# Optimization experiments

Hardware: AMD Instinct MI355X
Metric: run time of the kernel (lower is better)

## Reference

```python
import jax, jax.numpy as jnp
import numpy as np

B, P, D, A = 256, 196, 512, 512

def setup_inputs() -> dict:
    key = jax.random.key(0)
    ks = jax.random.split(key, 12)
    sc = 1.0 / np.sqrt(D)
    sa = 1.0 / np.sqrt(A)
    return {
        "encoder_out": jax.random.normal(ks[0], (B, P, D), jnp.float32),
        "decoder_hidden": jax.random.normal(ks[1], (B, D), jnp.float32),
        "st": jax.random.normal(ks[2], (B, D), jnp.float32),
        "Wv": jax.random.normal(ks[3], (D, A), jnp.float32) * sc,
        "bv": jnp.zeros((A,), jnp.float32),
        "Wh": jax.random.normal(ks[4], (D, A), jnp.float32) * sc,
        "bh": jnp.zeros((A,), jnp.float32),
        "Ws": jax.random.normal(ks[5], (D, A), jnp.float32) * sc,
        "bs": jnp.zeros((A,), jnp.float32),
        "Wav": jax.random.normal(ks[6], (A,), jnp.float32) * sa,
        "bav": jnp.zeros((), jnp.float32),
        "Was": jax.random.normal(ks[7], (A,), jnp.float32) * sa,
        "bas": jnp.zeros((), jnp.float32),
    }

def reference(encoder_out, decoder_hidden, st, Wv, bv, Wh, bh, Ws, bs, Wav, bav, Was, bas):
    # hidden: (B, A)
    hidden = decoder_hidden @ Wh + bh
    # v: (B, P, A)
    v = jnp.einsum('bpd,da->bpa', encoder_out, Wv) + bv
    # z_t: (B, P) -- additive attention scores over pixels
    z_t = jnp.einsum('bpa,a->bp', jnp.tanh(v + hidden[:, None, :]), Wav) + bav
    alpha_t = jax.nn.softmax(z_t, axis=1)
    # c_t: (B, D) -- attention-weighted encoding
    c_t = jnp.einsum('bpd,bp->bd', encoder_out, alpha_t)
    # sentinel branch: s (B, A), s_att (B, 1)
    s = st @ Ws + bs
    s_att = jnp.tanh(s + hidden) @ Was + bas  # (B,)
    z_t_extended = jnp.concatenate([z_t, s_att[:, None]], axis=1)  # (B, P+1)
    alpha_t_hat = jax.nn.softmax(z_t_extended, axis=1)
    beta_t = alpha_t_hat[:, -1:]  # (B, 1)
    c_hat_t = beta_t * st + (1.0 - beta_t) * c_t
    return (c_hat_t, alpha_t, beta_t)
```

## Files before the change

kernel.cpp:

```cpp
#include <hip/hip_runtime.h>
#include <hip/hip_bf16.h>
#include <cstdint>

#define B_ 256
#define P_ 196
#define D_ 512
#define A_ 512

#define OUT_CHAT  0
#define OUT_ALPHA (B_*D_)
#define OUT_BETA  (B_*D_ + B_*P_)

typedef unsigned short ushort_t;
typedef uint32_t u32;
typedef uint64_t u64;
typedef __attribute__((ext_vector_type(8))) __bf16 bf16x8;
typedef __attribute__((ext_vector_type(4))) float f32x4;

__device__ __forceinline__ ushort_t f2bf(float f) {
    union { float f; u32 i; } v; v.f = f;
    u32 r = (v.i + 0x7fffu + ((v.i >> 16) & 1u)) >> 16;
    return (ushort_t)r;
}
__device__ __forceinline__ float bfbits2f(u32 lo16) {
    union { u32 i; float f; } v; v.i = lo16 << 16; return v.f;
}
__device__ __forceinline__ u32 cvt2bf(float x, float y) {
    union { __hip_bfloat162 h; u32 u; } v;
    v.h = __float22bfloat162_rn(make_float2(x, y));
    return v.u;
}
__device__ __forceinline__ float tanh_fast(float x) {
    float e = __expf(2.0f * x);
    return 1.0f - 2.0f / (e + 1.0f);
}
__device__ __forceinline__ void async_load16(const ushort_t* g, ushort_t* l) {
    __builtin_amdgcn_global_load_lds(
        (const __attribute__((address_space(1))) unsigned int*)g,
        (__attribute__((address_space(3))) unsigned int*)l, 16, 0, 0);
}

__global__ __launch_bounds__(256) void k_prep(
    const float* __restrict__ E, const float* __restrict__ dh,
    const float* __restrict__ st,
    const float* __restrict__ Wv, const float* __restrict__ Wh,
    const float* __restrict__ Ws,
    ushort_t* __restrict__ Ebf, ushort_t* __restrict__ dhbf,
    ushort_t* __restrict__ stbf,
    ushort_t* __restrict__ WvT, ushort_t* __restrict__ WhT,
    ushort_t* __restrict__ WsT)
{
    __shared__ ushort_t tile[32][33];
    int bx = blockIdx.x;
    if (bx < 12544) {
        size_t i0 = (size_t)bx * 512 + threadIdx.x;
        const float4* src = (const float4*)E;
        u64* dst = (u64*)Ebf;
        float4 v0 = src[i0];
        float4 v1 = src[i0 + 256];
        dst[i0]       = (u64)cvt2bf(v0.x, v0.y) | ((u64)cvt2bf(v0.z, v0.w) << 32);
        dst[i0 + 256] = (u64)cvt2bf(v1.x, v1.y) | ((u64)cvt2bf(v1.z, v1.w) << 32);
    } else if (bx < 12672) {
        int gid = (bx - 12544) * 256 + threadIdx.x;
        float4 dv = ((const float4*)dh)[gid];
        float4 sv = ((const float4*)st)[gid];
        ((u64*)dhbf)[gid] = (u64)cvt2bf(dv.x, dv.y) | ((u64)cvt2bf(dv.z, dv.w) << 32);
        ((u64*)stbf)[gid] = (u64)cvt2bf(sv.x, sv.y) | ((u64)cvt2bf(sv.z, sv.w) << 32);
    } else {
        int idx = bx - 12672;
        int z   = idx >> 8;
        int rem = idx & 255;
        int tby = rem >> 4, tbx = rem & 15;
        const float* W  = (z == 0) ? Wv  : (z == 1) ? Wh  : Ws;
        ushort_t*    WT = (z == 0) ? WvT : (z == 1) ? WhT : WsT;
        int t = threadIdx.x, r = t >> 5, c = t & 31;
#pragma unroll
        for (int i = 0; i < 4; ++i) {
            int row = r + 8 * i;
            tile[row][c] = f2bf(W[(size_t)(tby * 32 + row) * A_ + tbx * 32 + c]);
        }
        __syncthreads();
#pragma unroll
        for (int i = 0; i < 4; ++i) {
            int row = r + 8 * i;
            WT[(size_t)(tbx * 32 + row) * D_ + tby * 32 + c] = tile[c][row];
        }
    }
}

#define PADK 72

__global__ __launch_bounds__(256) void k1_mfma(
    const ushort_t* __restrict__ dhbf, const ushort_t* __restrict__ stbf,
    const ushort_t* __restrict__ WhT,  const ushort_t* __restrict__ WsT,
    const float* __restrict__ bh, const float* __restrict__ bs,
    float* __restrict__ hidden_ws, float* __restrict__ s_ws)
{
    __shared__ ushort_t As[128 * PADK];
    __shared__ ushort_t Bs[128 * PADK];

    int mat = blockIdx.z;
    const ushort_t* Abf = mat ? stbf : dhbf;
    const ushort_t* WT  = mat ? WsT  : WhT;
    const float*    bia = mat ? bs   : bh;
    float*          outp = mat ? s_ws : hidden_ws;

    int tid = threadIdx.x;
    int m0 = blockIdx.y * 128;
    int n0 = blockIdx.x * 128;

    int lane = tid & 63, w = tid >> 6;
    int wm = w & 1, wn = w >> 1;
    int col = lane & 15, q = lane >> 4;

    f32x4 acc[4][4];
#pragma unroll
    for (int tm = 0; tm < 4; ++tm)
#pragma unroll
        for (int tn = 0; tn < 4; ++tn)
            acc[tm][tn] = (f32x4){0.f, 0.f, 0.f, 0.f};

    const ushort_t* arow = As + (wm * 64 + col) * PADK + q * 8;
    const ushort_t* brow = Bs + (wn * 64 + col) * PADK + q * 8;

    int sr = tid >> 3, sc = tid & 7;
    for (int kt = 0; kt < D_ / 64; ++kt) {
#pragma unroll
        for (int i = 0; i < 4; ++i) {
            int row = sr + i * 32;
            *(uint4*)(As + row * PADK + sc * 8) =
                *(const uint4*)(Abf + (size_t)(m0 + row) * D_ + kt * 64 + sc * 8);
            *(uint4*)(Bs + row * PADK + sc * 8) =
                *(const uint4*)(WT + (size_t)(n0 + row) * D_ + kt * 64 + sc * 8);
        }
        __syncthreads();
#pragma unroll
        for (int ks = 0; ks < 2; ++ks) {
            bf16x8 afr[4];
#pragma unroll
            for (int tm = 0; tm < 4; ++tm)
                afr[tm] = *(const bf16x8*)(arow + tm * 16 * PADK + ks * 32);
#pragma unroll
            for (int tn = 0; tn < 4; ++tn) {
                bf16x8 bfr = *(const bf16x8*)(brow + tn * 16 * PADK + ks * 32);
#pragma unroll
                for (int tm = 0; tm < 4; ++tm)
                    acc[tm][tn] = __builtin_amdgcn_mfma_f32_16x16x32_bf16(
                        afr[tm], bfr, acc[tm][tn], 0, 0, 0);
            }
        }
        __syncthreads();
    }

#pragma unroll
    for (int tm = 0; tm < 4; ++tm)
#pragma unroll
        for (int r = 0; r < 4; ++r) {
            int b = m0 + wm * 64 + tm * 16 + q * 4 + r;
#pragma unroll
            for (int tn = 0; tn < 4; ++tn) {
                int n = n0 + wn * 64 + tn * 16 + col;
                outp[(size_t)b * A_ + n] = acc[tm][tn][r] + bia[n];
            }
        }
}

#define BM 128
#define BN 256
#define BKk 64
__global__ __launch_bounds__(256, 3) void k2_z_bf(
    const ushort_t* __restrict__ Ebf, const ushort_t* __restrict__ WvT,
    const float* __restrict__ hidden_ws, const float* __restrict__ bv,
    const float* __restrict__ Wav, float* __restrict__ z2_ws)
{
    __shared__ ushort_t As[BM * BKk];
    __shared__ ushort_t Bs[BN * BKk];
    __shared__ float hv_s[2][BN];
    __shared__ float wav_s[BN];
    __shared__ float zpart[2][BM];

    int tid = threadIdx.x;
    int m0  = blockIdx.x * BM;
    int n0  = blockIdx.y * BN;
    int b0  = m0 / P_;
    int b1  = (m0 + BM - 1) / P_;

    {
        int a = n0 + tid;
        float bva = bv[a];
        hv_s[0][tid] = hidden_ws[(size_t)b0 * A_ + a] + bva;
        hv_s[1][tid] = hidden_ws[(size_t)b1 * A_ + a] + bva;
        wav_s[tid]   = Wav[a];
    }

    int lane = tid & 63, w = tid >> 6;
    int wm = w & 1, wn = w >> 1;
    int col = lane & 15, q = lane >> 4;

    f32x4 acc[4][8];
#pragma unroll
    for (int tm = 0; tm < 4; ++tm)
#pragma unroll
        for (int tn = 0; tn < 8; ++tn)
            acc[tm][tn] = (f32x4){0.f, 0.f, 0.f, 0.f};

    int srow = tid >> 3, spos = tid & 7;
    int gch  = spos ^ (srow & 7);
    const ushort_t* agb = Ebf + (size_t)(m0 + srow) * D_ + gch * 8;
    const ushort_t* bgb = WvT + (size_t)(n0 + srow) * D_ + gch * 8;
    ushort_t* alb = As + tid * 8;
    ushort_t* blb = Bs + tid * 8;

    int fx = col & 7;

    for (int kt = 0; kt < D_ / BKk; ++kt) {
#pragma unroll
        for (int i = 0; i < 4; ++i)
            async_load16(agb + (size_t)i * 32 * D_ + kt * BKk, alb + i * 2048);
#pragma unroll
        for (int i = 0; i < 8; ++i)
            async_load16(bgb + (size_t)i * 32 * D_ + kt * BKk, blb + i * 2048);
        __syncthreads();
#pragma unroll
        for (int ks = 0; ks < 2; ++ks) {
            bf16x8 afr[4];
#pragma unroll
            for (int tm = 0; tm < 4; ++tm)
                afr[tm] = *(const bf16x8*)(As + (wm * 64 + tm * 16 + col) * BKk
                                              + (((ks * 4 + q) ^ fx) * 8));
#pragma unroll
            for (int tn = 0; tn < 8; ++tn) {
                bf16x8 bfr = *(const bf16x8*)(Bs + (wn * 128 + tn * 16 + col) * BKk
                                                 + (((ks * 4 + q) ^ fx) * 8));
#pragma unroll
                for (int tm = 0; tm < 4; ++tm)
                    acc[tm][tn] = __builtin_amdgcn_mfma_f32_16x16x32_bf16(
                        afr[tm], bfr, acc[tm][tn], 0, 0, 0);
            }
        }
        __syncthreads();
    }

#pragma unroll
    for (int tm = 0; tm < 4; ++tm) {
#pragma unroll
        for (int r = 0; r < 4; ++r) {
            int row = wm * 64 + tm * 16 + q * 4 + r;
            int m   = m0 + row;
            int bsel = (m / P_) - b0;
            float zr = 0.f;
#pragma unroll
            for (int tn = 0; tn < 8; ++tn) {
                int nl = wn * 128 + tn * 16 + col;
                zr += wav_s[nl] * tanh_fast(acc[tm][tn][r] + hv_s[bsel][nl]);
            }
#pragma unroll
            for (int msk = 1; msk < 16; msk <<= 1)
                zr += __shfl_xor(zr, msk, 64);
            if (col == 0) zpart[wn][row] = zr;
        }
    }
    __syncthreads();
    if (tid < BM)
        z2_ws[(size_t)blockIdx.y * (B_ * P_) + m0 + tid] =
            zpart[0][tid] + zpart[1][tid];
}

__global__ __launch_bounds__(256) void k3_softmax(
    const float* __restrict__ z2_ws, const float* __restrict__ hidden_ws,
    const float* __restrict__ s_ws, const float* __restrict__ Was,
    const float* __restrict__ bas, const float* __restrict__ bav,
    float* __restrict__ alpha_ws, float* __restrict__ beta_ws,
    float* __restrict__ out)
{
    __shared__ float red[4];
    __shared__ float bm_s, bl_s, sa_s;
    int b = blockIdx.x, t = threadIdx.x;

    {
        int a0 = t, a1 = t + 256;
        float part = Was[a0] * tanh_fast(s_ws[(size_t)b * A_ + a0] + hidden_ws[(size_t)b * A_ + a0])
                   + Was[a1] * tanh_fast(s_ws[(size_t)b * A_ + a1] + hidden_ws[(size_t)b * A_ + a1]);
#pragma unroll
        for (int o = 32; o >= 1; o >>= 1) part += __shfl_down(part, o, 64);
        if ((t & 63) == 0) red[t >> 6] = part;
        __syncthreads();
        if (t == 0) sa_s = red[0] + red[1] + red[2] + red[3] + bas[0];
        __syncthreads();
    }

    float zv = (t < P_) ? (z2_ws[(size_t)b * P_ + t]
                         + z2_ws[(size_t)(B_ * P_) + (size_t)b * P_ + t] + bav[0])
                        : -1e30f;

    float m = zv;
#pragma unroll
    for (int o = 32; o >= 1; o >>= 1) m = fmaxf(m, __shfl_xor(m, o, 64));
    if ((t & 63) == 0) red[t >> 6] = m;
    __syncthreads();
    if (t == 0) bm_s = fmaxf(fmaxf(red[0], red[1]), fmaxf(red[2], red[3]));
    __syncthreads();
    float m1 = bm_s;

    float e = (t < P_) ? __expf(zv - m1) : 0.f;
    float s = e;
#pragma unroll
    for (int o = 32; o >= 1; o >>= 1) s += __shfl_xor(s, o, 64);
    if ((t & 63) == 0) red[t >> 6] = s;
    __syncthreads();
    if (t == 0) bl_s = red[0] + red[1] + red[2] + red[3];
    __syncthreads();
    float l1 = bl_s;

    if (t < P_) {
        float alpha = e / l1;
        alpha_ws[(size_t)b * P_ + t] = alpha;
        out[OUT_ALPHA + (size_t)b * P_ + t] = alpha;
    }
    float sa = sa_s;
    float m2 = fmaxf(m1, sa);
    float l2 = __expf(m1 - m2) * l1 + __expf(sa - m2);
    float beta = __expf(sa - m2) / l2;
    if (t == 0) {
        beta_ws[b] = beta;
        out[OUT_BETA + b] = beta;
    }
}

__global__ __launch_bounds__(256) void k4_final(
    const ushort_t* __restrict__ Ebf, const float* __restrict__ st,
    const float* __restrict__ alpha_ws, const float* __restrict__ beta_ws,
    float* __restrict__ out)
{
    __shared__ float al[P_];
    int b = blockIdx.x, t = threadIdx.x;
    if (t < P_) al[t] = alpha_ws[(size_t)b * P_ + t];
    __syncthreads();
    const u32* eb = (const u32*)(Ebf + (size_t)b * P_ * D_) + t;
    float a0 = 0.f, a1 = 0.f;
#pragma unroll 4
    for (int p = 0; p < P_; ++p) {
        u32 u = eb[(size_t)p * (D_ / 2)];
        float ap = al[p];
        a0 = fmaf(ap, bfbits2f(u & 0xffffu), a0);
        a1 = fmaf(ap, bfbits2f(u >> 16), a1);
    }
    float beta = beta_ws[b];
    float2 su = *(const float2*)(st + (size_t)b * D_ + 2 * t);
    float c0 = beta * su.x + (1.f - beta) * a0;
    float c1 = beta * su.y + (1.f - beta) * a1;
    *(float2*)(out + (size_t)b * D_ + 2 * t) = make_float2(c0, c1);
}

extern "C" void kernel_launch(void* const* d_in, const int* in_sizes, int n_in,
                              void* d_out, int out_size, void* d_ws, size_t ws_size,
                              hipStream_t stream)
{
    (void)in_sizes; (void)n_in; (void)out_size; (void)ws_size;
    const float* E   = (const float*)d_in[0];
    const float* dh  = (const float*)d_in[1];
    const float* st  = (const float*)d_in[2];
    const float* Wv  = (const float*)d_in[3];
    const float* bv  = (const float*)d_in[4];
    const float* Wh  = (const float*)d_in[5];
    const float* bh  = (const float*)d_in[6];
    const float* Ws  = (const float*)d_in[7];
    const float* bs  = (const float*)d_in[8];
    const float* Wav = (const float*)d_in[9];
    const float* bav = (const float*)d_in[10];
    const float* Was = (const float*)d_in[11];
    const float* bas = (const float*)d_in[12];
    float* out = (float*)d_out;

    char* ws = (char*)d_ws;
    ushort_t* WvT     = (ushort_t*)(ws);
    ushort_t* WhT     = (ushort_t*)(ws + 524288);
    ushort_t* WsT     = (ushort_t*)(ws + 1048576);
    float*    alpha_w = (float*)(ws + 1572864);
    float*    beta_w  = (float*)(ws + 1773568);
    float*    z2_w    = (float*)(ws + 1774592);
    ushort_t* dhbf    = (ushort_t*)(ws + 2176000);
    ushort_t* stbf    = (ushort_t*)(ws + 2438144);
    float*    hidden_w= (float*)(ws + 2700288);
    float*    s_w     = (float*)(ws + 3224576);
    ushort_t* Ebf     = (ushort_t*)(ws + 3748864);

    k_prep<<<12544 + 128 + 768, 256, 0, stream>>>(E, dh, st, Wv, Wh, Ws,
                                                  Ebf, dhbf, stbf, WvT, WhT, WsT);
    k1_mfma<<<dim3(4, 2, 2), 256, 0, stream>>>(dhbf, stbf, WhT, WsT, bh, bs,
                                               hidden_w, s_w);
    k2_z_bf<<<dim3((B_ * P_) / BM, A_ / BN), 256, 0, stream>>>(
        Ebf, WvT, hidden_w, bv, Wav, z2_w);
    k3_softmax<<<256, 256, 0, stream>>>(z2_w, hidden_w, s_w, Was, bas, bav,
                                        alpha_w, beta_w, out);
    k4_final<<<256, 256, 0, stream>>>(Ebf, st, alpha_w, beta_w, out);
}
```

Before: 258.8 us.

## Fuse softmax and context kernels, vectorize context loads, swizzle GEMM block order

Merges the softmax and weighted-context kernels into one 512-thread kernel that keeps alpha in shared memory. The alpha and beta round-trip through workspace and one launch go away. The context reduction now splits pixels across eight waves, each lane loading 16-byte chunks of bf16 rows, with a cross-wave reduction through shared memory. The GEMM kernel is also remapped to a 1D grid that interleaves the two N-halves of each M tile, aiming for better L2 reuse of the encoder rows.

```diff
diff --git a/kernel.cpp b/kernel.cpp
--- a/kernel.cpp
+++ b/kernel.cpp
@@ -38,6 +38,16 @@
     __builtin_amdgcn_global_load_lds(
         (const __attribute__((address_space(1))) unsigned int*)g,
         (__attribute__((address_space(3))) unsigned int*)l, 16, 0, 0);
+}
+__device__ __forceinline__ void fma8(float ap, uint4 v, float ac[8]) {
+    ac[0] = fmaf(ap, bfbits2f(v.x & 0xffffu), ac[0]);
+    ac[1] = fmaf(ap, bfbits2f(v.x >> 16),     ac[1]);
+    ac[2] = fmaf(ap, bfbits2f(v.y & 0xffffu), ac[2]);
+    ac[3] = fmaf(ap, bfbits2f(v.y >> 16),     ac[3]);
+    ac[4] = fmaf(ap, bfbits2f(v.z & 0xffffu), ac[4]);
+    ac[5] = fmaf(ap, bfbits2f(v.z >> 16),     ac[5]);
+    ac[6] = fmaf(ap, bfbits2f(v.w & 0xffffu), ac[6]);
+    ac[7] = fmaf(ap, bfbits2f(v.w >> 16),     ac[7]);
 }
 
 __global__ __launch_bounds__(256) void k_prep(
@@ -180,8 +190,11 @@
     __shared__ float zpart[2][BM];
 
     int tid = threadIdx.x;
-    int m0  = blockIdx.x * BM;
-    int n0  = blockIdx.y * BN;
+    int bx  = blockIdx.x;
+    int m_idx = ((bx >> 4) << 3) + (bx & 7);
+    int half  = (bx >> 3) & 1;
+    int m0  = m_idx * BM;
+    int n0  = half * BN;
     int b0  = m0 / P_;
     int b1  = (m0 + BM - 1) / P_;
 
@@ -262,94 +275,103 @@
     }
     __syncthreads();
     if (tid < BM)
-        z2_ws[(size_t)blockIdx.y * (B_ * P_) + m0 + tid] =
+        z2_ws[(size_t)half * (B_ * P_) + m0 + tid] =
             zpart[0][tid] + zpart[1][tid];
 }
 
-__global__ __launch_bounds__(256) void k3_softmax(
+__global__ __launch_bounds__(512) void k34_softmax_ct(
+    const ushort_t* __restrict__ Ebf, const float* __restrict__ st,
     const float* __restrict__ z2_ws, const float* __restrict__ hidden_ws,
     const float* __restrict__ s_ws, const float* __restrict__ Was,
     const float* __restrict__ bas, const float* __restrict__ bav,
-    float* __restrict__ alpha_ws, float* __restrict__ beta_ws,
     float* __restrict__ out)
 {
-    __shared__ float red[4];
+    __shared__ float red[8];
+    __shared__ float al[P_];
+    __shared__ float acc_s[8][516];
     __shared__ float bm_s, bl_s, sa_s;
+
     int b = blockIdx.x, t = threadIdx.x;
-
-    {
-        int a0 = t, a1 = t + 256;
-        float part = Was[a0] * tanh_fast(s_ws[(size_t)b * A_ + a0] + hidden_ws[(size_t)b * A_ + a0])
-                   + Was[a1] * tanh_fast(s_ws[(size_t)b * A_ + a1] + hidden_ws[(size_t)b * A_ + a1]);
-#pragma unroll
-        for (int o = 32; o >= 1; o >>= 1) part += __shfl_down(part, o, 64);
-        if ((t & 63) == 0) red[t >> 6] = part;
-        __syncthreads();
-        if (t == 0) sa_s = red[0] + red[1] + red[2] + red[3] + bas[0];
-        __syncthreads();
-    }
+    int lane = t & 63, w = t >> 6;
+
+    float part = Was[t] * tanh_fast(s_ws[(size_t)b * A_ + t]
+                                  + hidden_ws[(size_t)b * A_ + t]);
+#pragma unroll
+    for (int o = 32; o >= 1; o >>= 1) part += __shfl_down(part, o, 64);
+    if (lane == 0) red[w] = part;
+    __syncthreads();
+    if (t == 0) {
+        float s = 0.f;
+#pragma unroll
+        for (int i = 0; i < 8; ++i) s += red[i];
+        sa_s = s + bas[0];
+    }
+    __syncthreads();
 
     float zv = (t < P_) ? (z2_ws[(size_t)b * P_ + t]
                          + z2_ws[(size_t)(B_ * P_) + (size_t)b * P_ + t] + bav[0])
                         : -1e30f;
-
     float m = zv;
 #pragma unroll
     for (int o = 32; o >= 1; o >>= 1) m = fmaxf(m, __shfl_xor(m, o, 64));
-    if ((t & 63) == 0) red[t >> 6] = m;
-    __syncthreads();
-    if (t == 0) bm_s = fmaxf(fmaxf(red[0], red[1]), fmaxf(red[2], red[3]));
+    if (lane == 0) red[w] = m;
+    __syncthreads();
+    if (t == 0) {
+        float mm = red[0];
+#pragma unroll
+        for (int i = 1; i < 8; ++i) mm = fmaxf(mm, red[i]);
+        bm_s = mm;
+    }
     __syncthreads();
     float m1 = bm_s;
-
     float e = (t < P_) ? __expf(zv - m1) : 0.f;
     float s = e;
 #pragma unroll
     for (int o = 32; o >= 1; o >>= 1) s += __shfl_xor(s, o, 64);
-    if ((t & 63) == 0) red[t >> 6] = s;
-    __syncthreads();
-    if (t == 0) bl_s = red[0] + red[1] + red[2] + red[3];
+    if (lane == 0) red[w] = s;
+    __syncthreads();
+    if (t == 0) {
+        float ss = 0.f;
+#pragma unroll
+        for (int i = 0; i < 8; ++i) ss += red[i];
+        bl_s = ss;
+    }
     __syncthreads();
     float l1 = bl_s;
-
     if (t < P_) {
         float alpha = e / l1;
-        alpha_ws[(size_t)b * P_ + t] = alpha;
+        al[t] = alpha;
         out[OUT_ALPHA + (size_t)b * P_ + t] = alpha;
     }
     float sa = sa_s;
     float m2 = fmaxf(m1, sa);
-    float l2 = __expf(m1 - m2) * l1 + __expf(sa - m2);
-    float beta = __expf(sa - m2) / l2;
-    if (t == 0) {
-        beta_ws[b] = beta;
-        out[OUT_BETA + b] = beta;
-    }
-}
-
-__global__ __launch_bounds__(256) void k4_final(
-    const ushort_t* __restrict__ Ebf, const float* __restrict__ st,
-    const float* __restrict__ alpha_ws, const float* __restrict__ beta_ws,
-    float* __restrict__ out)
-{
-    __shared__ float al[P_];
-    int b = blockIdx.x, t = threadIdx.x;
-    if (t < P_) al[t] = alpha_ws[(size_t)b * P_ + t];
-    __syncthreads();
-    const u32* eb = (const u32*)(Ebf + (size_t)b * P_ * D_) + t;
-    float a0 = 0.f, a1 = 0.f;
+    float eb2 = __expf(sa - m2);
+    float l2 = __expf(m1 - m2) * l1 + eb2;
+    float beta = eb2 / l2;
+    if (t == 0) out[OUT_BETA + b] = beta;
+    __syncthreads();
+
+    float ac[8] = {0.f, 0.f, 0.f, 0.f, 0.f, 0.f, 0.f, 0.f};
+    const uint4* eb = (const uint4*)(Ebf + (size_t)b * P_ * D_);
 #pragma unroll 4
-    for (int p = 0; p < P_; ++p) {
-        u32 u = eb[(size_t)p * (D_ / 2)];
-        float ap = al[p];
-        a0 = fmaf(ap, bfbits2f(u & 0xffffu), a0);
-        a1 = fmaf(ap, bfbits2f(u >> 16), a1);
-    }
-    float beta = beta_ws[b];
-    float2 su = *(const float2*)(st + (size_t)b * D_ + 2 * t);
-    float c0 = beta * su.x + (1.f - beta) * a0;
-    float c1 = beta * su.y + (1.f - beta) * a1;
-    *(float2*)(out + (size_t)b * D_ + 2 * t) = make_float2(c0, c1);
+    for (int i = 0; i < 24; ++i) {
+        int pp = w + 8 * i;
+        uint4 v = eb[(size_t)pp * (D_ / 8) + lane];
+        fma8(al[pp], v, ac);
+    }
+    if (w < P_ - 192) {
+        int pp = 192 + w;
+        uint4 v = eb[(size_t)pp * (D_ / 8) + lane];
+        fma8(al[pp], v, ac);
+    }
+#pragma unroll
+    for (int j = 0; j < 8; ++j) acc_s[w][lane * 8 + j] = ac[j];
+    __syncthreads();
+    float c = 0.f;
+#pragma unroll
+    for (int g = 0; g < 8; ++g) c += acc_s[g][t];
+    float sv = st[(size_t)b * D_ + t];
+    out[OUT_CHAT + (size_t)b * D_ + t] = beta * sv + (1.f - beta) * c;
 }
 
 extern "C" void kernel_launch(void* const* d_in, const int* in_sizes, int n_in,
@@ -376,22 +398,18 @@
     ushort_t* WvT     = (ushort_t*)(ws);
     ushort_t* WhT     = (ushort_t*)(ws + 524288);
     ushort_t* WsT     = (ushort_t*)(ws + 1048576);
-    float*    alpha_w = (float*)(ws + 1572864);
-    float*    beta_w  = (float*)(ws + 1773568);
-    float*    z2_w    = (float*)(ws + 1774592);
-    ushort_t* dhbf    = (ushort_t*)(ws + 2176000);
-    ushort_t* stbf    = (ushort_t*)(ws + 2438144);
-    float*    hidden_w= (float*)(ws + 2700288);
-    float*    s_w     = (float*)(ws + 3224576);
-    ushort_t* Ebf     = (ushort_t*)(ws + 3748864);
+    float*    z2_w    = (float*)(ws + 1572864);
+    ushort_t* dhbf    = (ushort_t*)(ws + 1974272);
+    ushort_t* stbf    = (ushort_t*)(ws + 2236416);
+    float*    hidden_w= (float*)(ws + 2498560);
+    float*    s_w     = (float*)(ws + 3022848);
+    ushort_t* Ebf     = (ushort_t*)(ws + 3547136);
 
     k_prep<<<12544 + 128 + 768, 256, 0, stream>>>(E, dh, st, Wv, Wh, Ws,
                                                   Ebf, dhbf, stbf, WvT, WhT, WsT);
     k1_mfma<<<dim3(4, 2, 2), 256, 0, stream>>>(dhbf, stbf, WhT, WsT, bh, bs,
                                                hidden_w, s_w);
-    k2_z_bf<<<dim3((B_ * P_) / BM, A_ / BN), 256, 0, stream>>>(
-        Ebf, WvT, hidden_w, bv, Wav, z2_w);
-    k3_softmax<<<256, 256, 0, stream>>>(z2_w, hidden_w, s_w, Was, bas, bav,
-                                        alpha_w, beta_w, out);
-    k4_final<<<256, 256, 0, stream>>>(Ebf, st, alpha_w, beta_w, out);
-}
+    k2_z_bf<<<784, 256, 0, stream>>>(Ebf, WvT, hidden_w, bv, Wav, z2_w);
+    k34_softmax_ct<<<256, 512, 0, stream>>>(Ebf, st, z2_w, hidden_w, s_w,
+                                            Was, bas, bav, out);
+}
```

After: 251.3 us. -2.9%, faster.
